# Kernel tuning notes

Hardware: AMD Instinct MI355X
Metric: run time of the kernel (lower is better)

Reference implementation:

```python
import jax, jax.numpy as jnp
import numpy as np

MAX_DISTANCE = 50.0
NUM_BINS = 50
FEATURE_DIM = 64
B, K = 2048, 1024


def setup_inputs() -> dict:
    key = jax.random.key(0)
    k1, k2, k3, k4, k5, k6 = jax.random.split(key, 6)
    goal_positions = jax.random.normal(k1, (B, K, 2), dtype=jnp.float32) * 20.0
    ego_state = jax.random.normal(k2, (B, 4), dtype=jnp.float32)
    in_dim = NUM_BINS + 6  # 56
    s1 = 1.0 / np.sqrt(in_dim)
    s2 = 1.0 / np.sqrt(FEATURE_DIM)
    W1 = jax.random.uniform(k3, (in_dim, FEATURE_DIM), jnp.float32, -s1, s1)
    b1 = jax.random.uniform(k4, (FEATURE_DIM,), jnp.float32, -s1, s1)
    W2 = jax.random.uniform(k5, (FEATURE_DIM, 1), jnp.float32, -s2, s2)
    b2 = jax.random.uniform(k6, (1,), jnp.float32, -s2, s2)
    return {"goal_positions": goal_positions, "ego_state": ego_state,
            "W1": W1, "b1": b1, "W2": W2, "b2": b2}


def _histogram(goal_positions):
    # distances: (B, K); bin_idx = min(int(d / max_d * num_bins), num_bins - 1)
    d = jnp.linalg.norm(goal_positions, axis=-1)
    idx = jnp.floor(d / MAX_DISTANCE * NUM_BINS).astype(jnp.int32)
    idx = jnp.clip(idx, 0, NUM_BINS - 1)
    return jax.nn.one_hot(idx, NUM_BINS, dtype=goal_positions.dtype)  # (B, K, num_bins)


def reference(goal_positions, ego_state, W1, b1, W2, b2):
    hist = _histogram(goal_positions)                              # (B, K, nb)
    ego = jnp.broadcast_to(ego_state[:, None, :],
                           (goal_positions.shape[0], goal_positions.shape[1], 4))
    feats = jnp.concatenate([hist, goal_positions, ego], axis=-1)  # (B, K, nb+6)
    h = jax.nn.relu(jnp.einsum('bkf,fd->bkd', feats, W1) + b1)     # (B, K, feature_dim)
    scores = (jnp.einsum('bkd,do->bko', h, W2) + b2)[..., 0]       # (B, K)
    return scores
```

## Files before the change

kernel.cpp:

```cpp
#include <hip/hip_runtime.h>

#define NBIN 50
#define DIM  64
#define TPB  512

typedef float f32x2 __attribute__((ext_vector_type(2)));

__device__ __forceinline__ f32x2 pk_fma_vs(f32x2 v, f32x2 s, f32x2 c) {
    f32x2 r;
    asm("v_pk_fma_f32 %0, %1, %2, %3" : "=v"(r) : "v"(v), "s"(s), "v"(c));
    return r;
}
__device__ __forceinline__ f32x2 pk_fma_acc(f32x2 s, f32x2 t, f32x2 acc) {
    asm("v_pk_fma_f32 %0, %1, %2, %0" : "+v"(acc) : "s"(s), "v"(t));
    return acc;
}

__global__ __launch_bounds__(TPB, 8) void scorer_kernel(
    const float* __restrict__ goal,
    const float* __restrict__ ego,
    const float* __restrict__ W1,
    const float* __restrict__ b1,
    const float* __restrict__ W2,
    const float* __restrict__ b2,
    float* __restrict__ out)
{
    __shared__ float4 comb[16 * NBIN];

    const int b   = blockIdx.x;
    const int tid = threadIdx.x;

    const float4 g4 = ((const float4*)goal)[(size_t)b * (1024 / 2) + tid];
    const float4 eg = ((const float4*)ego)[b];

    const int   d  = tid & 63;
    const float ev = b1[d]
                   + eg.x * W1[52 * DIM + d]
                   + eg.y * W1[53 * DIM + d]
                   + eg.z * W1[54 * DIM + d]
                   + eg.w * W1[55 * DIM + d];

    const float2 p0 = make_float2(g4.x, g4.y);
    const float2 p1 = make_float2(g4.z, g4.w);
    int idx0, idx1;
    {
        float r2 = __fadd_rn(__fmul_rn(p0.x, p0.x), __fmul_rn(p0.y, p0.y));
        float fv = floorf(__fmul_rn(__fdiv_rn(__fsqrt_rn(r2), 50.0f), 50.0f));
        int ix = (int)fv;
        idx0 = ix < 0 ? 0 : (ix > NBIN - 1 ? NBIN - 1 : ix);
    }
    {
        float r2 = __fadd_rn(__fmul_rn(p1.x, p1.x), __fmul_rn(p1.y, p1.y));
        float fv = floorf(__fmul_rn(__fdiv_rn(__fsqrt_rn(r2), 50.0f), 50.0f));
        int ix = (int)fv;
        idx1 = ix < 0 ? 0 : (ix > NBIN - 1 ? NBIN - 1 : ix);
    }

    for (int i = tid; i < NBIN * DIM; i += TPB) {
        int bn = i >> 6;
        ((float*)comb)[((d >> 2) * NBIN + bn) * 4 + (d & 3)] = W1[i] + ev;
    }
    __syncthreads();

    const f32x2* w50v = (const f32x2*)(W1 + 50 * DIM);
    const f32x2* w51v = (const f32x2*)(W1 + 51 * DIM);
    const f32x2* w2v  = (const f32x2*)W2;
    const float  bias2 = b2[0];

    const f32x2 xx0 = {p0.x, p0.x}, yy0 = {p0.y, p0.y};
    const f32x2 xx1 = {p1.x, p1.x}, yy1 = {p1.y, p1.y};
    f32x2 a0l = {0.f, 0.f}, a0h = {0.f, 0.f};
    f32x2 a1l = {0.f, 0.f}, a1h = {0.f, 0.f};

#pragma unroll
    for (int d4 = 0; d4 < 16; ++d4) {
        const f32x2 wa0 = w50v[d4 * 2], wa1 = w50v[d4 * 2 + 1];
        const f32x2 wu0 = w51v[d4 * 2], wu1 = w51v[d4 * 2 + 1];
        const f32x2 wc0 = w2v[d4 * 2],  wc1 = w2v[d4 * 2 + 1];
        const float4 ga = comb[d4 * NBIN + idx0];
        const float4 gb = comb[d4 * NBIN + idx1];

        f32x2 t;
        t = pk_fma_vs(yy0, wu0, (f32x2){ga.x, ga.y});
        t = pk_fma_vs(xx0, wa0, t);
        t.x = fmaxf(t.x, 0.0f); t.y = fmaxf(t.y, 0.0f);
        a0l = pk_fma_acc(wc0, t, a0l);
        t = pk_fma_vs(yy0, wu1, (f32x2){ga.z, ga.w});
        t = pk_fma_vs(xx0, wa1, t);
        t.x = fmaxf(t.x, 0.0f); t.y = fmaxf(t.y, 0.0f);
        a0h = pk_fma_acc(wc1, t, a0h);
        t = pk_fma_vs(yy1, wu0, (f32x2){gb.x, gb.y});
        t = pk_fma_vs(xx1, wa0, t);
        t.x = fmaxf(t.x, 0.0f); t.y = fmaxf(t.y, 0.0f);
        a1l = pk_fma_acc(wc0, t, a1l);
        t = pk_fma_vs(yy1, wu1, (f32x2){gb.z, gb.w});
        t = pk_fma_vs(xx1, wa1, t);
        t.x = fmaxf(t.x, 0.0f); t.y = fmaxf(t.y, 0.0f);
        a1h = pk_fma_acc(wc1, t, a1h);
    }

    const float s0 = a0l.x + a0l.y + a0h.x + a0h.y + bias2;
    const float s1 = a1l.x + a1l.y + a1h.x + a1h.y + bias2;
    ((float2*)out)[(size_t)b * TPB + tid] = make_float2(s0, s1);
}

extern "C" void kernel_launch(void* const* d_in, const int* in_sizes, int n_in,
                              void* d_out, int out_size, void* d_ws, size_t ws_size,
                              hipStream_t stream) {
    const float* goal = (const float*)d_in[0];
    const float* ego  = (const float*)d_in[1];
    const float* W1   = (const float*)d_in[2];
    const float* b1   = (const float*)d_in[3];
    const float* W2   = (const float*)d_in[4];
    const float* b2   = (const float*)d_in[5];
    float* out = (float*)d_out;

    int B = in_sizes[1] / 4;
    scorer_kernel<<<dim3(B), dim3(TPB), 0, stream>>>(goal, ego, W1, b1, W2, b2, out);
}
```

Measured before the change: 23.58 us.

## Sort goals by bin within each wavefront to reduce LDS bank conflicts

Each thread now handles four goals instead of two, with 256 threads per block. For each goal slot, a 64-lane bitonic sort (DPP/swizzle) reorders lanes by histogram bin, so the LDS gathers from the combined W1 table hit fewer distinct addresses. The results are then permuted back to the original lanes with ds_permute. This adds about 21 compare-exchange steps plus shuffles per goal, which may cost more than the bank conflicts it removes.

```diff
diff --git a/kernel.cpp b/kernel.cpp
--- a/kernel.cpp
+++ b/kernel.cpp
@@ -2,7 +2,8 @@
 
 #define NBIN 50
 #define DIM  64
-#define TPB  512
+#define TPB  256
+#define KPT  4
 
 typedef float f32x2 __attribute__((ext_vector_type(2)));
 
@@ -16,7 +17,33 @@
     return acc;
 }
 
-__global__ __launch_bounds__(TPB, 8) void scorer_kernel(
+template <int J>
+__device__ __forceinline__ int xor_partner(int v) {
+    if constexpr (J == 1)  return __builtin_amdgcn_mov_dpp(v, 0xB1, 0xF, 0xF, false);
+    else if constexpr (J == 2)  return __builtin_amdgcn_mov_dpp(v, 0x4E, 0xF, 0xF, false);
+    else if constexpr (J == 32) return __shfl_xor(v, 32, 64);
+    else return __builtin_amdgcn_ds_swizzle(v, (J << 10) | 0x1F);
+}
+
+template <int K, int J>
+__device__ __forceinline__ void bstep(int& key, int lane) {
+    int partner = xor_partner<J>(key);
+    int mn = key < partner ? key : partner;
+    int mx = key < partner ? partner : key;
+    bool keep_small = ((lane & J) == 0) == ((lane & K) == 0);
+    key = keep_small ? mn : mx;
+}
+
+__device__ __forceinline__ void sort64(int& k, int lane) {
+    bstep<2, 1>(k, lane);
+    bstep<4, 2>(k, lane);  bstep<4, 1>(k, lane);
+    bstep<8, 4>(k, lane);  bstep<8, 2>(k, lane);  bstep<8, 1>(k, lane);
+    bstep<16, 8>(k, lane); bstep<16, 4>(k, lane); bstep<16, 2>(k, lane); bstep<16, 1>(k, lane);
+    bstep<32, 16>(k, lane); bstep<32, 8>(k, lane); bstep<32, 4>(k, lane); bstep<32, 2>(k, lane); bstep<32, 1>(k, lane);
+    bstep<64, 32>(k, lane); bstep<64, 16>(k, lane); bstep<64, 8>(k, lane); bstep<64, 4>(k, lane); bstep<64, 2>(k, lane); bstep<64, 1>(k, lane);
+}
+
+__global__ __launch_bounds__(TPB, 6) void scorer_kernel(
     const float* __restrict__ goal,
     const float* __restrict__ ego,
     const float* __restrict__ W1,
@@ -27,35 +54,29 @@
 {
     __shared__ float4 comb[16 * NBIN];
 
-    const int b   = blockIdx.x;
-    const int tid = threadIdx.x;
+    const int b    = blockIdx.x;
+    const int tid  = threadIdx.x;
+    const int lane = tid & 63;
 
-    const float4 g4 = ((const float4*)goal)[(size_t)b * (1024 / 2) + tid];
-    const float4 eg = ((const float4*)ego)[b];
+    const float2* gp = (const float2*)goal + (size_t)b * (TPB * KPT);
+    float2 p[KPT];
+    int    bin[KPT];
+#pragma unroll
+    for (int j = 0; j < KPT; ++j) {
+        p[j] = gp[j * TPB + tid];
+        float r2 = __fadd_rn(__fmul_rn(p[j].x, p[j].x), __fmul_rn(p[j].y, p[j].y));
+        float fv = floorf(__fmul_rn(__fdiv_rn(__fsqrt_rn(r2), 50.0f), 50.0f));
+        int ix = (int)fv;
+        bin[j] = ix < 0 ? 0 : (ix > NBIN - 1 ? NBIN - 1 : ix);
+    }
 
     const int   d  = tid & 63;
+    const float4 eg = ((const float4*)ego)[b];
     const float ev = b1[d]
                    + eg.x * W1[52 * DIM + d]
                    + eg.y * W1[53 * DIM + d]
                    + eg.z * W1[54 * DIM + d]
                    + eg.w * W1[55 * DIM + d];
-
-    const float2 p0 = make_float2(g4.x, g4.y);
-    const float2 p1 = make_float2(g4.z, g4.w);
-    int idx0, idx1;
-    {
-        float r2 = __fadd_rn(__fmul_rn(p0.x, p0.x), __fmul_rn(p0.y, p0.y));
-        float fv = floorf(__fmul_rn(__fdiv_rn(__fsqrt_rn(r2), 50.0f), 50.0f));
-        int ix = (int)fv;
-        idx0 = ix < 0 ? 0 : (ix > NBIN - 1 ? NBIN - 1 : ix);
-    }
-    {
-        float r2 = __fadd_rn(__fmul_rn(p1.x, p1.x), __fmul_rn(p1.y, p1.y));
-        float fv = floorf(__fmul_rn(__fdiv_rn(__fsqrt_rn(r2), 50.0f), 50.0f));
-        int ix = (int)fv;
-        idx1 = ix < 0 ? 0 : (ix > NBIN - 1 ? NBIN - 1 : ix);
-    }
-
     for (int i = tid; i < NBIN * DIM; i += TPB) {
         int bn = i >> 6;
         ((float*)comb)[((d >> 2) * NBIN + bn) * 4 + (d & 3)] = W1[i] + ev;
@@ -67,41 +88,38 @@
     const f32x2* w2v  = (const f32x2*)W2;
     const float  bias2 = b2[0];
 
-    const f32x2 xx0 = {p0.x, p0.x}, yy0 = {p0.y, p0.y};
-    const f32x2 xx1 = {p1.x, p1.x}, yy1 = {p1.y, p1.y};
-    f32x2 a0l = {0.f, 0.f}, a0h = {0.f, 0.f};
-    f32x2 a1l = {0.f, 0.f}, a1h = {0.f, 0.f};
+#pragma unroll
+    for (int j = 0; j < KPT; ++j) {
+        int key = (bin[j] << 6) | lane;
+        sort64(key, lane);
+        const int origin = key & 63;
+        const int sbin   = key >> 6;
+        const float xs = __shfl(p[j].x, origin, 64);
+        const float ys = __shfl(p[j].y, origin, 64);
 
+        const f32x2 xx = {xs, xs}, yy = {ys, ys};
+        f32x2 al = {0.f, 0.f}, ah = {0.f, 0.f};
 #pragma unroll
-    for (int d4 = 0; d4 < 16; ++d4) {
-        const f32x2 wa0 = w50v[d4 * 2], wa1 = w50v[d4 * 2 + 1];
-        const f32x2 wu0 = w51v[d4 * 2], wu1 = w51v[d4 * 2 + 1];
-        const f32x2 wc0 = w2v[d4 * 2],  wc1 = w2v[d4 * 2 + 1];
-        const float4 ga = comb[d4 * NBIN + idx0];
-        const float4 gb = comb[d4 * NBIN + idx1];
+        for (int d4 = 0; d4 < 16; ++d4) {
+            const f32x2 wa0 = w50v[d4 * 2], wa1 = w50v[d4 * 2 + 1];
+            const f32x2 wu0 = w51v[d4 * 2], wu1 = w51v[d4 * 2 + 1];
+            const f32x2 wc0 = w2v[d4 * 2],  wc1 = w2v[d4 * 2 + 1];
+            const float4 g = comb[d4 * NBIN + sbin];
+            f32x2 t;
+            t = pk_fma_vs(yy, wu0, (f32x2){g.x, g.y});
+            t = pk_fma_vs(xx, wa0, t);
+            t.x = fmaxf(t.x, 0.0f); t.y = fmaxf(t.y, 0.0f);
+            al = pk_fma_acc(wc0, t, al);
+            t = pk_fma_vs(yy, wu1, (f32x2){g.z, g.w});
+            t = pk_fma_vs(xx, wa1, t);
+            t.x = fmaxf(t.x, 0.0f); t.y = fmaxf(t.y, 0.0f);
+            ah = pk_fma_acc(wc1, t, ah);
+        }
+        float s = al.x + al.y + ah.x + ah.y + bias2;
 
-        f32x2 t;
-        t = pk_fma_vs(yy0, wu0, (f32x2){ga.x, ga.y});
-        t = pk_fma_vs(xx0, wa0, t);
-        t.x = fmaxf(t.x, 0.0f); t.y = fmaxf(t.y, 0.0f);
-        a0l = pk_fma_acc(wc0, t, a0l);
-        t = pk_fma_vs(yy0, wu1, (f32x2){ga.z, ga.w});
-        t = pk_fma_vs(xx0, wa1, t);
-        t.x = fmaxf(t.x, 0.0f); t.y = fmaxf(t.y, 0.0f);
-        a0h = pk_fma_acc(wc1, t, a0h);
-        t = pk_fma_vs(yy1, wu0, (f32x2){gb.x, gb.y});
-        t = pk_fma_vs(xx1, wa0, t);
-        t.x = fmaxf(t.x, 0.0f); t.y = fmaxf(t.y, 0.0f);
-        a1l = pk_fma_acc(wc0, t, a1l);
-        t = pk_fma_vs(yy1, wu1, (f32x2){gb.z, gb.w});
-        t = pk_fma_vs(xx1, wa1, t);
-        t.x = fmaxf(t.x, 0.0f); t.y = fmaxf(t.y, 0.0f);
-        a1h = pk_fma_acc(wc1, t, a1h);
+        int sb = __builtin_amdgcn_ds_permute(origin << 2, __float_as_int(s));
+        out[(size_t)b * (TPB * KPT) + j * TPB + tid] = __int_as_float(sb);
     }
-
-    const float s0 = a0l.x + a0l.y + a0h.x + a0h.y + bias2;
-    const float s1 = a1l.x + a1l.y + a1h.x + a1h.y + bias2;
-    ((float2*)out)[(size_t)b * TPB + tid] = make_float2(s0, s1);
 }
 
 extern "C" void kernel_launch(void* const* d_in, const int* in_sizes, int n_in,
```

After: 29.90 us. 1.27x slower.
